# Kernel optimization log

Hardware: AMD Instinct MI355X
Metric: run time of the kernel (lower is better)

Reference implementation:

```python
import jax, jax.numpy as jnp
import numpy as np

TOP_K = 16  # init kwarg top_k


def setup_inputs() -> dict:
    key = jax.random.key(0)
    ks = jax.random.split(key, 10)
    B, N = 4, 4096
    p = lambda k, shape: jax.random.normal(k, shape, jnp.float32) * 0.05
    return {
        "s": jax.random.normal(ks[0], (B, N, 4), jnp.float32),
        "g": jax.random.normal(ks[1], (B, N, 2), jnp.float32),
        # edge MLP (1x1 convs): 5 -> 64 -> 128  (5 = 4 rel-state + eye flag)
        "w1": p(ks[2], (64, 5)),   "b1": jnp.zeros((64,), jnp.float32),
        "w2": p(ks[3], (128, 64)), "b2": jnp.zeros((128,), jnp.float32),
        # node MLP: 132 -> 64 -> 128 -> 64 -> 4  (132 = 128 pooled + 2 pos-goal + 2 vel)
        "fw1": p(ks[4], (64, 132)), "fb1": jnp.zeros((64,), jnp.float32),
        "fw2": p(ks[5], (128, 64)), "fb2": jnp.zeros((128,), jnp.float32),
        "fw3": p(ks[6], (64, 128)), "fb3": jnp.zeros((64,), jnp.float32),
        "fw4": p(ks[7], (4, 64)),   "fb4": jnp.zeros((4,), jnp.float32),
    }


def reference(s, g, w1, b1, w2, b2, fw1, fb1, fw2, fb2, fw3, fb3, fw4, fb4):
    B, N, D = s.shape
    pos = s[..., :2]                                   # [B,N,2]
    # squared pairwise distances without materializing [B,N,N,2]
    sq = jnp.sum(pos * pos, axis=-1)                   # [B,N]
    d2 = sq[:, :, None] + sq[:, None, :] - 2.0 * jnp.einsum('bnd,bmd->bnm', pos, pos)
    # top_k NEAREST neighbors (includes self, dist 0)
    _, idx = jax.lax.top_k(-d2, TOP_K)                 # idx: [B,N,K]
    # gather neighbor states per batch (avoids [B,N,N,D] blowup)
    nbr = jax.vmap(lambda sb, ib: sb[ib])(s, idx)      # [B,N,K,D]
    rel = s[:, :, None, :] - nbr                       # relative state
    eye = (idx == jnp.arange(N)[None, :, None]).astype(s.dtype)[..., None]
    e = jnp.concatenate([rel, eye], axis=-1)           # [B,N,K,5]
    # shared edge MLP (conv1x1 equivalents)
    h = jax.nn.relu(jnp.einsum('bnkc,oc->bnko', e, w1) + b1)
    h = jax.nn.relu(jnp.einsum('bnkc,oc->bnko', h, w2) + b2)
    feat = jnp.max(h, axis=2)                          # max-pool over neighbors -> [B,N,128]
    node = jnp.concatenate([feat, pos - g, s[..., 2:]], axis=-1)  # [B,N,132]
    h = jax.nn.relu(node @ fw1.T + fb1)
    h = jax.nn.relu(h @ fw2.T + fb2)
    h = jax.nn.relu(h @ fw3.T + fb3)
    out = h @ fw4.T + fb4
    return 2.0 * jax.nn.sigmoid(out) - 1.0             # [B,N,4]
```

## Files before the change

### kernel.cpp

```cpp
#include <hip/hip_runtime.h>
#include <math.h>

#define NPT 4096
#define NTOT 16384

__global__ __launch_bounds__(256) void k0_u(const float* __restrict__ s,
                                            const float* __restrict__ w1,
                                            float* __restrict__ u,
                                            float* __restrict__ w14) {
  int gid = blockIdx.x * 256 + threadIdx.x;
  int n = gid >> 4;
  int c0 = (gid & 15) << 2;
  float4 sv = *(const float4*)(s + (size_t)n * 4);
  float uv[4];
#pragma unroll
  for (int i = 0; i < 4; ++i) {
    const float* wr = w1 + (size_t)(c0 + i) * 5;
    uv[i] = wr[0] * sv.x + wr[1] * sv.y + wr[2] * sv.z + wr[3] * sv.w;
  }
  float4 o; o.x = uv[0]; o.y = uv[1]; o.z = uv[2]; o.w = uv[3];
  *(float4*)(u + (size_t)n * 64 + c0) = o;
  if (blockIdx.x == 0 && threadIdx.x < 64)
    w14[threadIdx.x] = w1[threadIdx.x * 5 + 4];
}

__global__ __launch_bounds__(256) void k1_knn(const float* __restrict__ s,
                                              unsigned short* __restrict__ knn) {
  const int tid = threadIdx.x;
  const int lane = tid & 63;
  const int row = blockIdx.x * 4 + (tid >> 6);
  const int b = row >> 12, n = row & 4095;
  const float* sb = s + (size_t)b * NPT * 4;
  const float2 pn = *(const float2*)(sb + (size_t)n * 4);
  const float sqn = pn.x * pn.x + pn.y * pn.y;
  const float INF = __builtin_inff();

  float d2v[64];
  float m1v = INF, m2v = INF;
  int m1s = 0, m2s = 0;
#pragma unroll
  for (int i = 0; i < 64; ++i) {
    const int m = i * 64 + lane;
    float2 pm = *(const float2*)(sb + (size_t)m * 4);
    float sqm = pm.x * pm.x + pm.y * pm.y;
    float dot = pn.x * pm.x + pn.y * pm.y;
    float d2 = (sqn + sqm) - 2.f * dot;
    d2v[i] = d2;
    bool c1 = d2 < m1v;
    bool c2 = d2 < m2v;
    m2v = c1 ? m1v : (c2 ? d2 : m2v);
    m2s = c1 ? m1s : (c2 ? i : m2s);
    m1v = c1 ? d2 : m1v;
    m1s = c1 ? i : m1s;
  }

  float lval = m1v;
  int lm = m1s * 64 + lane;
  bool have2 = true;
  unsigned long long emask = 0;

  for (int r = 0; r < 16; ++r) {
    float wv = lval; int wm = lm;
#pragma unroll
    for (int off = 32; off >= 1; off >>= 1) {
      float ov = __shfl_xor(wv, off, 64);
      int   om = __shfl_xor(wm, off, 64);
      bool bet = (ov < wv) || (ov == wv && om < wm);
      wv = bet ? ov : wv;
      wm = bet ? om : wm;
    }
    if (lane == r) knn[(size_t)row * 16 + r] = (unsigned short)wm;
    if ((wm & 63) == lane) {
      emask |= 1ull << (wm >> 6);
      if (have2) {
        lval = m2v; lm = m2s * 64 + lane; have2 = false;
      } else {
        float bv = INF; int bs = 0;
#pragma unroll
        for (int i = 0; i < 64; ++i) {
          bool sk = (emask >> i) & 1ull;
          bool bet2 = (!sk) && (d2v[i] < bv);
          bv = bet2 ? d2v[i] : bv;
          bs = bet2 ? i : bs;
        }
        lval = bv; lm = bs * 64 + lane;
      }
    }
  }
}

#define DOT4ACC(acc, hv, wv) \
  acc = fmaf((hv).x, (wv).x, fmaf((hv).y, (wv).y, fmaf((hv).z, (wv).z, fmaf((hv).w, (wv).w, acc))))

__global__ __launch_bounds__(256) void k2_edge(
    const float* __restrict__ s, const float* __restrict__ g,
    const float* __restrict__ b1, const float* __restrict__ w2g,
    const float* __restrict__ b2, const float* __restrict__ u,
    const float* __restrict__ w14, const unsigned short* __restrict__ knn,
    float* __restrict__ node) {
  __shared__ float h1T[128 * 68];
  __shared__ float w2T[128 * 68];
  const int tid = threadIdx.x;

  for (int gi = tid; gi < 2048; gi += 256) {
    int o = gi >> 4, ct = gi & 15;
    float4 v = *(const float4*)(w2g + (size_t)gi * 4);
    *(float4*)(w2T + o * 68 + ct * 4) = v;
  }

  {
    const int row = tid >> 1, half = tid & 1, c0 = half * 32;
    const int p = row >> 4, k = row & 15;
    const int n_pt = blockIdx.x * 8 + p;
    const int n_in = n_pt & 4095;
    const int base_b = n_pt - n_in;
    int m_in = knn[(size_t)n_pt * 16 + k] & 4095;
    const float eye = (m_in == n_in) ? 1.f : 0.f;
    const float* un = u + (size_t)n_pt * 64 + c0;
    const float* um = u + (size_t)(base_b + m_in) * 64 + c0;
#pragma unroll
    for (int t = 0; t < 8; ++t) {
      float4 a   = *(const float4*)(un + t * 4);
      float4 bb  = *(const float4*)(um + t * 4);
      float4 b1v = *(const float4*)(b1 + c0 + t * 4);
      float4 wv  = *(const float4*)(w14 + c0 + t * 4);
      float4 h;
      h.x = fmaxf(fmaf(eye, wv.x, (a.x + b1v.x) - bb.x), 0.f);
      h.y = fmaxf(fmaf(eye, wv.y, (a.y + b1v.y) - bb.y), 0.f);
      h.z = fmaxf(fmaf(eye, wv.z, (a.z + b1v.z) - bb.z), 0.f);
      h.w = fmaxf(fmaf(eye, wv.w, (a.w + b1v.w) - bb.w), 0.f);
      *(float4*)(h1T + row * 68 + c0 + t * 4) = h;
    }
  }
  __syncthreads();

  {
    const int p = tid >> 5, oh = tid & 31;
    const int n_pt = blockIdx.x * 8 + p;
    float4 acc[16];
    float4 binit;
    binit.x = b2[oh]; binit.y = b2[oh + 32]; binit.z = b2[oh + 64]; binit.w = b2[oh + 96];
#pragma unroll
    for (int kk = 0; kk < 16; ++kk) acc[kk] = binit;

#pragma unroll 4
    for (int ct = 0; ct < 16; ++ct) {
      float4 w0 = *(const float4*)(w2T + (oh      ) * 68 + ct * 4);
      float4 w1v = *(const float4*)(w2T + (oh + 32) * 68 + ct * 4);
      float4 w2v = *(const float4*)(w2T + (oh + 64) * 68 + ct * 4);
      float4 w3v = *(const float4*)(w2T + (oh + 96) * 68 + ct * 4);
#pragma unroll
      for (int kk = 0; kk < 16; ++kk) {
        float4 hv = *(const float4*)(h1T + (p * 16 + kk) * 68 + ct * 4);
        DOT4ACC(acc[kk].x, hv, w0);
        DOT4ACC(acc[kk].y, hv, w1v);
        DOT4ACC(acc[kk].z, hv, w2v);
        DOT4ACC(acc[kk].w, hv, w3v);
      }
    }
    float4 f = acc[0];
#pragma unroll
    for (int kk = 1; kk < 16; ++kk) {
      f.x = fmaxf(f.x, acc[kk].x); f.y = fmaxf(f.y, acc[kk].y);
      f.z = fmaxf(f.z, acc[kk].z); f.w = fmaxf(f.w, acc[kk].w);
    }
    f.x = fmaxf(f.x, 0.f); f.y = fmaxf(f.y, 0.f);
    f.z = fmaxf(f.z, 0.f); f.w = fmaxf(f.w, 0.f);
    float* nrow = node + (size_t)n_pt * 132;
    nrow[oh] = f.x; nrow[oh + 32] = f.y; nrow[oh + 64] = f.z; nrow[oh + 96] = f.w;
    if (oh == 0) {
      float4 sv = *(const float4*)(s + (size_t)n_pt * 4);
      float2 gv = *(const float2*)(g + (size_t)n_pt * 2);
      nrow[128] = sv.x - gv.x; nrow[129] = sv.y - gv.y;
      nrow[130] = sv.z; nrow[131] = sv.w;
    }
  }
}

__global__ __launch_bounds__(256) void k3_node(
    const float* __restrict__ node,
    const float* __restrict__ fw1, const float* __restrict__ fb1,
    const float* __restrict__ fw2, const float* __restrict__ fb2,
    const float* __restrict__ fw3, const float* __restrict__ fb3,
    const float* __restrict__ fw4, const float* __restrict__ fb4,
    float* __restrict__ out) {
  __shared__ float bufA[32 * 136];
  __shared__ float bufB[32 * 136];
  __shared__ float wb[64 * 136];
  const int tid = threadIdx.x;
  const int n0 = blockIdx.x * 32;
  const int p = tid >> 3, og = tid & 7;

  for (int gi = tid; gi < 32 * 33; gi += 256) {
    int r = gi / 33, ct = gi - r * 33;
    *(float4*)(bufA + r * 136 + ct * 4) = *(const float4*)(node + (size_t)(n0 + r) * 132 + ct * 4);
  }
  for (int gi = tid; gi < 64 * 33; gi += 256) {
    int r = gi / 33, ct = gi - r * 33;
    *(float4*)(wb + r * 136 + ct * 4) = *(const float4*)(fw1 + (size_t)r * 132 + ct * 4);
  }
  __syncthreads();

  {
    float acc[8];
#pragma unroll
    for (int j = 0; j < 8; ++j) acc[j] = fb1[og + 8 * j];
    for (int ct = 0; ct < 33; ++ct) {
      float4 in4 = *(const float4*)(bufA + p * 136 + ct * 4);
#pragma unroll
      for (int j = 0; j < 8; ++j) {
        float4 w4 = *(const float4*)(wb + (og + 8 * j) * 136 + ct * 4);
        DOT4ACC(acc[j], in4, w4);
      }
    }
#pragma unroll
    for (int j = 0; j < 8; ++j) bufB[p * 136 + og + 8 * j] = fmaxf(acc[j], 0.f);
  }
  __syncthreads();
  for (int gi = tid; gi < 128 * 16; gi += 256) {
    int r = gi >> 4, ct = gi & 15;
    *(float4*)(wb + r * 68 + ct * 4) = *(const float4*)(fw2 + (size_t)r * 64 + ct * 4);
  }
  __syncthreads();

  {
    float acc[16];
#pragma unroll
    for (int j = 0; j < 16; ++j) acc[j] = fb2[og + 8 * j];
    for (int ct = 0; ct < 16; ++ct) {
      float4 in4 = *(const float4*)(bufB + p * 136 + ct * 4);
#pragma unroll
      for (int j = 0; j < 16; ++j) {
        float4 w4 = *(const float4*)(wb + (og + 8 * j) * 68 + ct * 4);
        DOT4ACC(acc[j], in4, w4);
      }
    }
#pragma unroll
    for (int j = 0; j < 16; ++j) bufA[p * 136 + og + 8 * j] = fmaxf(acc[j], 0.f);
  }
  __syncthreads();
  for (int gi = tid; gi < 64 * 32; gi += 256) {
    int r = gi >> 5, ct = gi & 31;
    *(float4*)(wb + r * 132 + ct * 4) = *(const float4*)(fw3 + (size_t)r * 128 + ct * 4);
  }
  __syncthreads();

  {
    float acc[8];
#pragma unroll
    for (int j = 0; j < 8; ++j) acc[j] = fb3[og + 8 * j];
    for (int ct = 0; ct < 32; ++ct) {
      float4 in4 = *(const float4*)(bufA + p * 136 + ct * 4);
#pragma unroll
      for (int j = 0; j < 8; ++j) {
        float4 w4 = *(const float4*)(wb + (og + 8 * j) * 132 + ct * 4);
        DOT4ACC(acc[j], in4, w4);
      }
    }
#pragma unroll
    for (int j = 0; j < 8; ++j) bufB[p * 136 + og + 8 * j] = fmaxf(acc[j], 0.f);
  }
  __syncthreads();
  for (int gi = tid; gi < 4 * 16; gi += 256) {
    int r = gi >> 4, ct = gi & 15;
    *(float4*)(wb + r * 68 + ct * 4) = *(const float4*)(fw4 + (size_t)r * 64 + ct * 4);
  }
  __syncthreads();

  if (tid < 128) {
    const int pp = tid >> 2, o = tid & 3;
    float acc = fb4[o];
    for (int ct = 0; ct < 16; ++ct) {
      float4 in4 = *(const float4*)(bufB + pp * 136 + ct * 4);
      float4 w4 = *(const float4*)(wb + o * 68 + ct * 4);
      DOT4ACC(acc, in4, w4);
    }
    float sgm = 1.f / (1.f + expf(-acc));
    out[(size_t)(n0 + pp) * 4 + o] = fmaf(2.f, sgm, -1.f);
  }
}

extern "C" void kernel_launch(void* const* d_in, const int* in_sizes, int n_in,
                              void* d_out, int out_size, void* d_ws, size_t ws_size,
                              hipStream_t stream) {
  (void)in_sizes; (void)n_in; (void)out_size; (void)ws_size;
  const float* s   = (const float*)d_in[0];
  const float* g   = (const float*)d_in[1];
  const float* w1  = (const float*)d_in[2];
  const float* b1  = (const float*)d_in[3];
  const float* w2  = (const float*)d_in[4];
  const float* b2  = (const float*)d_in[5];
  const float* fw1 = (const float*)d_in[6];
  const float* fb1 = (const float*)d_in[7];
  const float* fw2 = (const float*)d_in[8];
  const float* fb2 = (const float*)d_in[9];
  const float* fw3 = (const float*)d_in[10];
  const float* fb3 = (const float*)d_in[11];
  const float* fw4 = (const float*)d_in[12];
  const float* fb4 = (const float*)d_in[13];

  float* ws   = (float*)d_ws;
  float* u    = ws;
  float* w14  = ws + 1048576;
  unsigned short* knn16 = (unsigned short*)(ws + 1048576 + 64);
  float* node = ws + 1048576 + 64 + 131072;
  float* out  = (float*)d_out;

  k0_u   <<<1024, 256, 0, stream>>>(s, w1, u, w14);
  k1_knn <<<4096, 256, 0, stream>>>(s, knn16);
  k2_edge<<<2048, 256, 0, stream>>>(s, g, b1, w2, b2, u, w14, knn16, node);
  k3_node<<<512,  256, 0, stream>>>(node, fw1, fb1, fw2, fb2, fw3, fb3, fw4, fb4, out);
}
```

Measured before the change: 259.4 us.

## Stage KNN positions in LDS, recompute distances, pack key+index for shuffle argmin

The KNN kernel now loads each batch's xy positions into shared memory once per block and reads candidates from LDS instead of global memory. It no longer keeps a 64-entry per-lane distance array in registers. When a lane has to refill beyond its two cached minima, it recomputes distances from LDS. The shuffle argmin packs an order-preserving float key and the index into one 64-bit value, so each step needs a single compare. This cuts register pressure and global loads, which should help occupancy, at the cost of a 32KB LDS staging per block and occasional recomputation.

```diff
diff --git a/kernel.cpp b/kernel.cpp
--- a/kernel.cpp
+++ b/kernel.cpp
@@ -24,28 +24,39 @@
     w14[threadIdx.x] = w1[threadIdx.x * 5 + 4];
 }
 
+__device__ __forceinline__ unsigned int fkey(float f) {
+  unsigned int u = __float_as_uint(f);
+  return u ^ ((unsigned int)((int)u >> 31) | 0x80000000u);
+}
+
 __global__ __launch_bounds__(256) void k1_knn(const float* __restrict__ s,
                                               unsigned short* __restrict__ knn) {
+  __shared__ float2 xy[NPT];
   const int tid = threadIdx.x;
   const int lane = tid & 63;
   const int row = blockIdx.x * 4 + (tid >> 6);
   const int b = row >> 12, n = row & 4095;
   const float* sb = s + (size_t)b * NPT * 4;
-  const float2 pn = *(const float2*)(sb + (size_t)n * 4);
+  const float INF = __builtin_inff();
+
+#pragma unroll
+  for (int j = 0; j < 16; ++j) {
+    int idx = tid + j * 256;
+    xy[idx] = *(const float2*)(sb + (size_t)idx * 4);
+  }
+  __syncthreads();
+
+  const float2 pn = xy[n];
   const float sqn = pn.x * pn.x + pn.y * pn.y;
-  const float INF = __builtin_inff();
-
-  float d2v[64];
+
   float m1v = INF, m2v = INF;
   int m1s = 0, m2s = 0;
-#pragma unroll
+#pragma unroll 8
   for (int i = 0; i < 64; ++i) {
-    const int m = i * 64 + lane;
-    float2 pm = *(const float2*)(sb + (size_t)m * 4);
+    float2 pm = xy[i * 64 + lane];
     float sqm = pm.x * pm.x + pm.y * pm.y;
     float dot = pn.x * pm.x + pn.y * pm.y;
     float d2 = (sqn + sqm) - 2.f * dot;
-    d2v[i] = d2;
     bool c1 = d2 < m1v;
     bool c2 = d2 < m2v;
     m2v = c1 ? m1v : (c2 ? d2 : m2v);
@@ -54,36 +65,40 @@
     m1s = c1 ? i : m1s;
   }
 
-  float lval = m1v;
-  int lm = m1s * 64 + lane;
+  unsigned long long lkey =
+      ((unsigned long long)fkey(m1v) << 32) | (unsigned)(m1s * 64 + lane);
+  unsigned long long k2b =
+      ((unsigned long long)fkey(m2v) << 32) | (unsigned)(m2s * 64 + lane);
   bool have2 = true;
   unsigned long long emask = 0;
 
   for (int r = 0; r < 16; ++r) {
-    float wv = lval; int wm = lm;
+    unsigned long long wk = lkey;
 #pragma unroll
     for (int off = 32; off >= 1; off >>= 1) {
-      float ov = __shfl_xor(wv, off, 64);
-      int   om = __shfl_xor(wm, off, 64);
-      bool bet = (ov < wv) || (ov == wv && om < wm);
-      wv = bet ? ov : wv;
-      wm = bet ? om : wm;
-    }
-    if (lane == r) knn[(size_t)row * 16 + r] = (unsigned short)wm;
-    if ((wm & 63) == lane) {
-      emask |= 1ull << (wm >> 6);
+      unsigned long long ok =
+          (unsigned long long)__shfl_xor((long long)wk, off, 64);
+      wk = (ok < wk) ? ok : wk;
+    }
+    unsigned int m = (unsigned int)wk & 4095u;
+    if (lane == r) knn[(size_t)row * 16 + r] = (unsigned short)m;
+    if ((int)((unsigned int)wk & 63u) == lane) {
+      emask |= 1ull << (m >> 6);
       if (have2) {
-        lval = m2v; lm = m2s * 64 + lane; have2 = false;
+        lkey = k2b; have2 = false;
       } else {
         float bv = INF; int bs = 0;
-#pragma unroll
         for (int i = 0; i < 64; ++i) {
-          bool sk = (emask >> i) & 1ull;
-          bool bet2 = (!sk) && (d2v[i] < bv);
-          bv = bet2 ? d2v[i] : bv;
-          bs = bet2 ? i : bs;
+          if ((emask >> i) & 1ull) continue;
+          float2 pm = xy[i * 64 + lane];
+          float sqm = pm.x * pm.x + pm.y * pm.y;
+          float dot = pn.x * pm.x + pn.y * pm.y;
+          float d2 = (sqn + sqm) - 2.f * dot;
+          bool bet = d2 < bv;
+          bv = bet ? d2 : bv;
+          bs = bet ? i : bs;
         }
-        lval = bv; lm = bs * 64 + lane;
+        lkey = ((unsigned long long)fkey(bv) << 32) | (unsigned)(bs * 64 + lane);
       }
     }
   }
```

Result: slower. 290.7 us (+12.1%).
